# Kernel optimization log

Hardware: AMD Instinct MI355X
Metric: run time of the kernel (lower is better)

Reference implementation:

```python
import jax, jax.numpy as jnp
import numpy as np

N, F_IN, HID, E = 100000, 128, 64, 3200000


def setup_inputs() -> dict:
    key = jax.random.key(0)
    ks = jax.random.split(key, 12)
    s = 0.05
    inp = {
        "x": jax.random.normal(ks[0], (N, F_IN), jnp.float32),
        "edge_index": jax.random.randint(ks[1], (2, E), 0, N, dtype=jnp.int32),
        "edge_weight": jax.random.uniform(ks[2], (E,), jnp.float32),
    }
    C = F_IN + HID  # DConv input channels = cat([X, H])
    # DConv weights have shape (2, K, in_channels, out_channels); K = 1 here.
    inp["Wz"] = s * jax.random.normal(ks[3], (2, 1, C, HID), jnp.float32)
    inp["bz"] = jnp.zeros((HID,), jnp.float32)
    inp["Wr"] = s * jax.random.normal(ks[4], (2, 1, C, HID), jnp.float32)
    inp["br"] = jnp.zeros((HID,), jnp.float32)
    inp["Wh"] = s * jax.random.normal(ks[5], (2, 1, C, HID), jnp.float32)
    inp["bh"] = jnp.zeros((HID,), jnp.float32)
    inp["Wlin"] = s * jax.random.normal(ks[6], (HID, 1), jnp.float32)
    inp["blin"] = jnp.zeros((1,), jnp.float32)
    return inp


def _dconv_k1(Y, W, b):
    # DConv with K=1: only the 0-th Chebyshev term of both diffusion
    # directions is used -> Y @ (W[0,0] + W[1,0]) + b. No propagation.
    return jnp.matmul(Y, W[0, 0] + W[1, 0]) + b


def reference(x, edge_index, edge_weight, Wz, bz, Wr, br, Wh, bh, Wlin, blin):
    n = x.shape[0]
    # Faithful-but-unused: original DConv normalizes edge weights by
    # out/in degree before the K>1 check; with K=1 it never affects output.
    row, col = edge_index[0], edge_index[1]
    deg_out = jax.ops.segment_sum(edge_weight, row, num_segments=n)
    deg_in = jax.ops.segment_sum(edge_weight, col, num_segments=n)
    _norm_out = jnp.where(deg_out[row] > 0, edge_weight / deg_out[row], 0.0)
    _norm_in = jnp.where(deg_in[col] > 0, edge_weight / deg_in[col], 0.0)

    H0 = jnp.zeros((n, Wz.shape[-1]), x.dtype)  # _set_hidden_state -> zeros
    XH = jnp.concatenate([x, H0], axis=1)       # [N, F_IN + HID]
    Z = jax.nn.sigmoid(_dconv_k1(XH, Wz, bz))   # update gate
    R = jax.nn.sigmoid(_dconv_k1(XH, Wr, br))   # reset gate
    XRH = jnp.concatenate([x, R * H0], axis=1)
    H_tilde = jnp.tanh(_dconv_k1(XRH, Wh, bh))
    H = Z * H0 + (1.0 - Z) * H_tilde            # GRU state update

    h = jax.nn.relu(H)
    # dropout: identity in eval mode (deterministic reference)
    return jnp.matmul(h, Wlin) + blin            # [N, 1]
```

## Files before the change

kernel.cpp:

```cpp
#include <hip/hip_runtime.h>
#include <hip/hip_bf16.h>

using bf16x8 = __attribute__((ext_vector_type(8))) short;
using f32x4  = __attribute__((ext_vector_type(4))) float;

static constexpr int kN          = 100000;
static constexpr int kFIN        = 128;
static constexpr int kTermStride = 192 * 64;
static constexpr int kTiles      = kN / 16;
static constexpr int kBlocks     = 512;
static constexpr int kWavesTot   = kBlocks * 8;
static constexpr int kExtra      = kTiles - kWavesTot;

__device__ __forceinline__ short f2bf(float v) {
    union { float f; unsigned u; } a; a.f = v;
    unsigned r = a.u + 0x7fffu + ((a.u >> 16) & 1u);
    return (short)(r >> 16);
}

__device__ __forceinline__ unsigned cvt_pk_bf16(float a, float b) {
    unsigned r;
    asm("v_cvt_pk_bf16_f32 %0, %1, %2" : "=v"(r) : "v"(a), "v"(b));
    return r;
}

__device__ __forceinline__ float rcp_fast(float x) { return __builtin_amdgcn_rcpf(x); }
__device__ __forceinline__ float sigmoid_fast(float x) {
    return rcp_fast(1.0f + __expf(-x));
}
__device__ __forceinline__ float tanh_fast(float x) {
    float e = __expf(2.0f * x);
    return 1.0f - 2.0f * rcp_fast(e + 1.0f);
}

__device__ __forceinline__ float row16_sum(float v) {
    int x;
    x = __builtin_amdgcn_update_dpp(0, __float_as_int(v), 0x128, 0xF, 0xF, false);
    v += __int_as_float(x);
    x = __builtin_amdgcn_update_dpp(0, __float_as_int(v), 0x124, 0xF, 0xF, false);
    v += __int_as_float(x);
    x = __builtin_amdgcn_update_dpp(0, __float_as_int(v), 0x122, 0xF, 0xF, false);
    v += __int_as_float(x);
    x = __builtin_amdgcn_update_dpp(0, __float_as_int(v), 0x121, 0xF, 0xF, false);
    v += __int_as_float(x);
    return v;
}

__global__ __launch_bounds__(512, 4) void fused_gcn(
    const float* __restrict__ x,
    const float* __restrict__ Wz,
    const float* __restrict__ bz,
    const float* __restrict__ Wh,
    const float* __restrict__ bh,
    const float* __restrict__ wlin,
    const float* __restrict__ blin,
    float* __restrict__ out)
{
    __shared__ short lw[16384];

    const int t    = threadIdx.x;
    const int wid  = t >> 6;
    const int lane = t & 63;
    const int r    = lane & 15;
    const int g    = lane >> 4;
    const int gw   = blockIdx.x * 8 + wid;
    const int t0   = gw;
    const int t1   = (gw < kExtra) ? kWavesTot + gw : -1;

    f32x4 f[8];
    auto load_x = [&](int tile) {
        const float* xrow = x + (size_t)(tile * 16 + r) * kFIN;
        #pragma unroll
        for (int kk = 0; kk < 4; ++kk) {
            f[kk * 2]     = *(const f32x4*)(xrow + kk * 32 + g * 8);
            f[kk * 2 + 1] = *(const f32x4*)(xrow + kk * 32 + g * 8 + 4);
        }
    };

    load_x(t0);

    float bzc[4], bhc[4], wlc[4];
    #pragma unroll
    for (int jt = 0; jt < 4; ++jt) {
        int c = jt * 16 + r;
        bzc[jt] = bz[c]; bhc[jt] = bh[c]; wlc[jt] = wlin[c];
    }
    const float bl = blin[0];

    {
        const int s   = t >> 4;
        const int jtp = (t >> 2) & 3;
        const int base_rt = jtp * 512 + (s >> 3) * 128 + (s & 7);
        short* dst[4];
        #pragma unroll
        for (int i = 0; i < 4; ++i) {
            const int cl = (t & 3) * 4 + i;
            dst[i] = &lw[base_rt + ((cl ^ jtp) << 3)];
        }
        #pragma unroll
        for (int mat = 0; mat < 2; ++mat) {
            const float* W = mat ? Wh : Wz;
            #pragma unroll
            for (int it = 0; it < 4; ++it) {
                const int fidx = it * 2048 + t * 4;
                f32x4 w0 = *(const f32x4*)(W + fidx);
                f32x4 w1 = *(const f32x4*)(W + kTermStride + fidx);
                const int cmi = mat * 8192 + it * 2048;
                #pragma unroll
                for (int i = 0; i < 4; ++i)
                    dst[i][cmi] = f2bf(w0[i] + w1[i]);
            }
        }
    }
    __syncthreads();

    int lx[4];
    #pragma unroll
    for (int jt = 0; jt < 4; ++jt) lx[jt] = ((lane ^ jt) << 3);

    bf16x8 a[4];
    auto cvt = [&]() {
        #pragma unroll
        for (int kk = 0; kk < 4; ++kk) {
            union { unsigned u[4]; bf16x8 v; } p;
            p.u[0] = cvt_pk_bf16(f[kk * 2][0], f[kk * 2][1]);
            p.u[1] = cvt_pk_bf16(f[kk * 2][2], f[kk * 2][3]);
            p.u[2] = cvt_pk_bf16(f[kk * 2 + 1][0], f[kk * 2 + 1][1]);
            p.u[3] = cvt_pk_bf16(f[kk * 2 + 1][2], f[kk * 2 + 1][3]);
            a[kk] = p.v;
        }
    };

    auto compute_tile = [&](int tile) {
        f32x4 accz[4], acch[4];
        #pragma unroll
        for (int jt = 0; jt < 4; ++jt) {
            accz[jt] = f32x4{0.f, 0.f, 0.f, 0.f};
            acch[jt] = f32x4{0.f, 0.f, 0.f, 0.f};
        }
        #pragma unroll
        for (int kk = 0; kk < 4; ++kk) {
            #pragma unroll
            for (int jt = 0; jt < 4; ++jt) {
                const int off = ((kk * 4 + jt) << 9) + lx[jt];
                bf16x8 wz = *(const bf16x8*)&lw[off];
                bf16x8 wh = *(const bf16x8*)&lw[8192 + off];
                accz[jt] = __builtin_amdgcn_mfma_f32_16x16x32_bf16(a[kk], wz, accz[jt], 0, 0, 0);
                acch[jt] = __builtin_amdgcn_mfma_f32_16x16x32_bf16(a[kk], wh, acch[jt], 0, 0, 0);
            }
        }
        float contrib[4] = {0.f, 0.f, 0.f, 0.f};
        #pragma unroll
        for (int jt = 0; jt < 4; ++jt) {
            #pragma unroll
            for (int i = 0; i < 4; ++i) {
                float z  = sigmoid_fast(accz[jt][i] + bzc[jt]);
                float ht = tanh_fast(acch[jt][i] + bhc[jt]);
                float H  = (1.0f - z) * ht;
                contrib[i] += fmaxf(H, 0.f) * wlc[jt];
            }
        }
        #pragma unroll
        for (int i = 0; i < 4; ++i) contrib[i] = row16_sum(contrib[i]);
        if (r == 0) {
            f32x4 o;
            #pragma unroll
            for (int i = 0; i < 4; ++i) o[i] = contrib[i] + bl;
            *(f32x4*)(out + tile * 16 + g * 4) = o;
        }
    };

    cvt();
    if (t1 >= 0) load_x(t1);
    compute_tile(t0);
    if (t1 >= 0) {
        cvt();
        compute_tile(t1);
    }
}

extern "C" void kernel_launch(void* const* d_in, const int* in_sizes, int n_in,
                              void* d_out, int out_size, void* d_ws, size_t ws_size,
                              hipStream_t stream) {
    const float* x    = (const float*)d_in[0];
    const float* Wz   = (const float*)d_in[3];
    const float* bz   = (const float*)d_in[4];
    const float* Wh   = (const float*)d_in[7];
    const float* bh   = (const float*)d_in[8];
    const float* wlin = (const float*)d_in[9];
    const float* blin = (const float*)d_in[10];

    fused_gcn<<<dim3(kBlocks), dim3(512), 0, stream>>>(
        x, Wz, bz, Wh, bh, wlin, blin, (float*)d_out);
}
```

Baseline: 18.94 us.

## Switch to 32x32x16 MFMA with one 32-row tile per wave

Replaces the 16x16x32 bf16 MFMA path, which gave each wave up to two 16-row tiles, with 32x32x16 MFMA on a single 32-row tile per wave. The LDS weight layout is reorganised to feed the B operand of the larger MFMA, and the epilogue reduction adds a cross-half shuffle. The goal is fewer LDS reads per FLOP, fewer MFMA issues and no serial second-tile phase. In exchange it uses larger accumulators, so register pressure rises, and 3125 waves leave some of the 4096 launched waves idle.

```diff
diff --git a/kernel.cpp b/kernel.cpp
--- a/kernel.cpp
+++ b/kernel.cpp
@@ -3,14 +3,13 @@
 
 using bf16x8 = __attribute__((ext_vector_type(8))) short;
 using f32x4  = __attribute__((ext_vector_type(4))) float;
+using f32x16 = __attribute__((ext_vector_type(16))) float;
 
 static constexpr int kN          = 100000;
 static constexpr int kFIN        = 128;
 static constexpr int kTermStride = 192 * 64;
-static constexpr int kTiles      = kN / 16;
+static constexpr int kTiles32    = kN / 32;
 static constexpr int kBlocks     = 512;
-static constexpr int kWavesTot   = kBlocks * 8;
-static constexpr int kExtra      = kTiles - kWavesTot;
 
 __device__ __forceinline__ short f2bf(float v) {
     union { float f; unsigned u; } a; a.f = v;
@@ -61,42 +60,34 @@
     const int t    = threadIdx.x;
     const int wid  = t >> 6;
     const int lane = t & 63;
-    const int r    = lane & 15;
-    const int g    = lane >> 4;
+    const int r32  = lane & 31;
+    const int hi   = lane >> 5;
     const int gw   = blockIdx.x * 8 + wid;
-    const int t0   = gw;
-    const int t1   = (gw < kExtra) ? kWavesTot + gw : -1;
+    const bool active = gw < kTiles32;
 
-    f32x4 f[8];
-    auto load_x = [&](int tile) {
-        const float* xrow = x + (size_t)(tile * 16 + r) * kFIN;
+    f32x4 f[16];
+    if (active) {
+        const float* xrow = x + (size_t)(gw * 32 + r32) * kFIN;
         #pragma unroll
-        for (int kk = 0; kk < 4; ++kk) {
-            f[kk * 2]     = *(const f32x4*)(xrow + kk * 32 + g * 8);
-            f[kk * 2 + 1] = *(const f32x4*)(xrow + kk * 32 + g * 8 + 4);
+        for (int k2 = 0; k2 < 8; ++k2) {
+            f[k2 * 2]     = *(const f32x4*)(xrow + k2 * 16 + hi * 8);
+            f[k2 * 2 + 1] = *(const f32x4*)(xrow + k2 * 16 + hi * 8 + 4);
         }
-    };
+    }
 
-    load_x(t0);
-
-    float bzc[4], bhc[4], wlc[4];
+    float bzc[2], bhc[2], wlc[2];
     #pragma unroll
-    for (int jt = 0; jt < 4; ++jt) {
-        int c = jt * 16 + r;
+    for (int jt = 0; jt < 2; ++jt) {
+        int c = jt * 32 + r32;
         bzc[jt] = bz[c]; bhc[jt] = bh[c]; wlc[jt] = wlin[c];
     }
     const float bl = blin[0];
 
     {
-        const int s   = t >> 4;
-        const int jtp = (t >> 2) & 3;
-        const int base_rt = jtp * 512 + (s >> 3) * 128 + (s & 7);
-        short* dst[4];
-        #pragma unroll
-        for (int i = 0; i < 4; ++i) {
-            const int cl = (t & 3) * 4 + i;
-            dst[i] = &lw[base_rt + ((cl ^ jtp) << 3)];
-        }
+        const int s    = t >> 4;
+        const int jtw  = (t & 15) >> 3;
+        const int base = ((s >> 3) & 1) * 256 + ((t & 7) * 4) * 8 + (s & 7)
+                       + jtw * 512;
         #pragma unroll
         for (int mat = 0; mat < 2; ++mat) {
             const float* W = mat ? Wh : Wz;
@@ -105,77 +96,71 @@
                 const int fidx = it * 2048 + t * 4;
                 f32x4 w0 = *(const f32x4*)(W + fidx);
                 f32x4 w1 = *(const f32x4*)(W + kTermStride + fidx);
-                const int cmi = mat * 8192 + it * 2048;
+                const int kap = it * 2 + (s >> 4);
+                const int d0  = mat * 8192 + kap * 1024 + base;
                 #pragma unroll
                 for (int i = 0; i < 4; ++i)
-                    dst[i][cmi] = f2bf(w0[i] + w1[i]);
+                    lw[d0 + i * 8] = f2bf(w0[i] + w1[i]);
             }
         }
     }
     __syncthreads();
+    if (!active) return;
 
-    int lx[4];
+    bf16x8 a[8];
     #pragma unroll
-    for (int jt = 0; jt < 4; ++jt) lx[jt] = ((lane ^ jt) << 3);
+    for (int k2 = 0; k2 < 8; ++k2) {
+        union { unsigned u[4]; bf16x8 v; } p;
+        p.u[0] = cvt_pk_bf16(f[k2 * 2][0], f[k2 * 2][1]);
+        p.u[1] = cvt_pk_bf16(f[k2 * 2][2], f[k2 * 2][3]);
+        p.u[2] = cvt_pk_bf16(f[k2 * 2 + 1][0], f[k2 * 2 + 1][1]);
+        p.u[3] = cvt_pk_bf16(f[k2 * 2 + 1][2], f[k2 * 2 + 1][3]);
+        a[k2] = p.v;
+    }
 
-    bf16x8 a[4];
-    auto cvt = [&]() {
+    f32x16 accz0, accz1, acch0, acch1;
+    #pragma unroll
+    for (int q = 0; q < 16; ++q) {
+        accz0[q] = 0.f; accz1[q] = 0.f; acch0[q] = 0.f; acch1[q] = 0.f;
+    }
+    const int rdbase = hi * 256 + r32 * 8;
+    #pragma unroll
+    for (int k2 = 0; k2 < 8; ++k2) {
+        const short* pz = &lw[k2 * 1024 + rdbase];
+        bf16x8 wz0 = *(const bf16x8*)(pz);
+        bf16x8 wz1 = *(const bf16x8*)(pz + 512);
+        bf16x8 wh0 = *(const bf16x8*)(pz + 8192);
+        bf16x8 wh1 = *(const bf16x8*)(pz + 8704);
+        accz0 = __builtin_amdgcn_mfma_f32_32x32x16_bf16(a[k2], wz0, accz0, 0, 0, 0);
+        accz1 = __builtin_amdgcn_mfma_f32_32x32x16_bf16(a[k2], wz1, accz1, 0, 0, 0);
+        acch0 = __builtin_amdgcn_mfma_f32_32x32x16_bf16(a[k2], wh0, acch0, 0, 0, 0);
+        acch1 = __builtin_amdgcn_mfma_f32_32x32x16_bf16(a[k2], wh1, acch1, 0, 0, 0);
+    }
+
+    float contrib[16];
+    #pragma unroll
+    for (int j = 0; j < 16; ++j) {
+        float z0 = sigmoid_fast(accz0[j] + bzc[0]);
+        float h0 = tanh_fast(acch0[j] + bhc[0]);
+        float v  = fmaxf((1.0f - z0) * h0, 0.f) * wlc[0];
+        float z1 = sigmoid_fast(accz1[j] + bzc[1]);
+        float h1 = tanh_fast(acch1[j] + bhc[1]);
+        v       += fmaxf((1.0f - z1) * h1, 0.f) * wlc[1];
+        contrib[j] = v;
+    }
+    #pragma unroll
+    for (int j = 0; j < 16; ++j) {
+        contrib[j] = row16_sum(contrib[j]);
+        contrib[j] += __shfl_xor(contrib[j], 16, 64);
+    }
+    if (r32 == 0) {
         #pragma unroll
-        for (int kk = 0; kk < 4; ++kk) {
-            union { unsigned u[4]; bf16x8 v; } p;
-            p.u[0] = cvt_pk_bf16(f[kk * 2][0], f[kk * 2][1]);
-            p.u[1] = cvt_pk_bf16(f[kk * 2][2], f[kk * 2][3]);
-            p.u[2] = cvt_pk_bf16(f[kk * 2 + 1][0], f[kk * 2 + 1][1]);
-            p.u[3] = cvt_pk_bf16(f[kk * 2 + 1][2], f[kk * 2 + 1][3]);
-            a[kk] = p.v;
-        }
-    };
-
-    auto compute_tile = [&](int tile) {
-        f32x4 accz[4], acch[4];
-        #pragma unroll
-        for (int jt = 0; jt < 4; ++jt) {
-            accz[jt] = f32x4{0.f, 0.f, 0.f, 0.f};
-            acch[jt] = f32x4{0.f, 0.f, 0.f, 0.f};
-        }
-        #pragma unroll
-        for (int kk = 0; kk < 4; ++kk) {
-            #pragma unroll
-            for (int jt = 0; jt < 4; ++jt) {
-                const int off = ((kk * 4 + jt) << 9) + lx[jt];
-                bf16x8 wz = *(const bf16x8*)&lw[off];
-                bf16x8 wh = *(const bf16x8*)&lw[8192 + off];
-                accz[jt] = __builtin_amdgcn_mfma_f32_16x16x32_bf16(a[kk], wz, accz[jt], 0, 0, 0);
-                acch[jt] = __builtin_amdgcn_mfma_f32_16x16x32_bf16(a[kk], wh, acch[jt], 0, 0, 0);
-            }
-        }
-        float contrib[4] = {0.f, 0.f, 0.f, 0.f};
-        #pragma unroll
-        for (int jt = 0; jt < 4; ++jt) {
-            #pragma unroll
-            for (int i = 0; i < 4; ++i) {
-                float z  = sigmoid_fast(accz[jt][i] + bzc[jt]);
-                float ht = tanh_fast(acch[jt][i] + bhc[jt]);
-                float H  = (1.0f - z) * ht;
-                contrib[i] += fmaxf(H, 0.f) * wlc[jt];
-            }
-        }
-        #pragma unroll
-        for (int i = 0; i < 4; ++i) contrib[i] = row16_sum(contrib[i]);
-        if (r == 0) {
+        for (int b = 0; b < 4; ++b) {
             f32x4 o;
             #pragma unroll
-            for (int i = 0; i < 4; ++i) o[i] = contrib[i] + bl;
-            *(f32x4*)(out + tile * 16 + g * 4) = o;
+            for (int q = 0; q < 4; ++q) o[q] = contrib[b * 4 + q] + bl;
+            *(f32x4*)(out + gw * 32 + b * 8 + hi * 4) = o;
         }
-    };
-
-    cvt();
-    if (t1 >= 0) load_x(t1);
-    compute_tile(t0);
-    if (t1 >= 0) {
-        cvt();
-        compute_tile(t1);
     }
 }
 
```

Measured after the change: 21.19 us. +11.9%, slower.
